# Optimization experiments

Hardware: AMD Instinct MI355X
Metric: run time of the kernel (lower is better)

The kernel has to match this reference:

```python
import jax, jax.numpy as jnp
import numpy as np

B, F, DU, DI, DT = 4096, 50, 128, 256, 768
NU, NI = 200000, 100000
EPS = 1e-5

def _batchnorm(x, gamma, beta):
    # training-mode BatchNorm1d: biased batch statistics
    mu = jnp.mean(x, axis=0)
    var = jnp.mean((x - mu) ** 2, axis=0)
    return gamma * (x - mu) / jnp.sqrt(var + EPS) + beta

def setup_inputs() -> dict:
    key = jax.random.key(0)
    ks = jax.random.split(key, 16)
    inp = {
        "user_id": jax.random.randint(ks[0], (B,), 0, NU),
        "item_id": jax.random.randint(ks[1], (B,), 0, NI),
        "user_follow": jax.random.randint(ks[2], (B, F), 0, NU),
        "follow_len": jax.random.randint(ks[3], (B,), 0, F + 1),
        "feature_item": jax.random.normal(ks[4], (B, 3), dtype=jnp.float32),
        "tag_emb": jax.random.normal(ks[5], (B, DT), dtype=jnp.float32),
        "user_emb_table": jax.random.normal(ks[6], (NU, DU), dtype=jnp.float32) * 0.02,
        "item_emb_table": jax.random.normal(ks[7], (NI, DI), dtype=jnp.float32) * 0.02,
        "fc1_w": jax.random.normal(ks[8], (DI, DT + DI), dtype=jnp.float32) * 0.02,
        "fc1_b": jnp.zeros((DI,), dtype=jnp.float32),
        "fc2_w": jax.random.normal(ks[9], (DU, DU + DI), dtype=jnp.float32) * 0.02,
        "fc2_b": jnp.zeros((DU,), dtype=jnp.float32),
        "out_w": jax.random.normal(ks[10], (1, DU + 3), dtype=jnp.float32) * 0.02,
        "out_b": jnp.zeros((1,), dtype=jnp.float32),
        "bn1_g": jnp.ones((DI,), dtype=jnp.float32),
        "bn1_b": jnp.zeros((DI,), dtype=jnp.float32),
        "bn2_g": jnp.ones((DU,), dtype=jnp.float32),
        "bn2_b": jnp.zeros((DU,), dtype=jnp.float32),
    }
    return inp

def reference(user_id, item_id, user_follow, follow_len, feature_item, tag_emb,
              user_emb_table, item_emb_table, fc1_w, fc1_b, fc2_w, fc2_b,
              out_w, out_b, bn1_g, bn1_b, bn2_g, bn2_b):
    # --- user interaction embedding (vectorized padded attention) ---
    u = user_emb_table[user_id]                       # [B, 128]
    f = user_emb_table[user_follow]                   # [B, F, 128]
    uf = jnp.concatenate([u[:, None, :], f], axis=1)  # [B, 1+F, 128]
    scores = jnp.einsum('bnd,bd->bn', uf, u)          # [B, 1+F]
    pos_valid = jnp.arange(F)[None, :] < follow_len[:, None]
    valid = jnp.concatenate([jnp.ones((user_id.shape[0], 1), dtype=bool), pos_valid], axis=1)
    scores = jnp.where(valid, scores, -1e9)
    w = jax.nn.softmax(scores, axis=1)
    att = jnp.einsum('bn,bnd->bd', w, uf)             # [B, 128]
    user_embedded = jnp.where((follow_len > 1)[:, None], att, u)
    # --- item fusion path ---
    item_embedded = item_emb_table[item_id]           # [B, 256]
    h1 = jnp.concatenate([tag_emb, item_embedded], axis=1) @ fc1_w.T + fc1_b
    item_vector = jax.nn.relu(_batchnorm(h1 + item_embedded, bn1_g, bn1_b))
    h2 = jnp.concatenate([user_embedded, item_vector], axis=1) @ fc2_w.T + fc2_b
    item_user_vector = jax.nn.relu(_batchnorm(h2 + user_embedded, bn2_g, bn2_b))
    logits = jnp.concatenate([item_user_vector, feature_item], axis=1) @ out_w.T + out_b
    return logits
```

## Files before the change

### kernel.cpp

```cpp
#include <hip/hip_runtime.h>
#include <cstdint>
#include <cstddef>

#define BATCH 4096
#define F_FOLLOW 50
#define NROW 51
#define DU 128
#define DI 256
#define DT 768
#define K1 (DT + DI)
#define K2 (DU + DI)
#define EPS 1e-5f

__global__ __launch_bounds__(256) void attn_kernel(
    const int* __restrict__ user_id,
    const int* __restrict__ user_follow,
    const int* __restrict__ follow_len,
    const float* __restrict__ utab,
    float* __restrict__ uemb_out,
    float* __restrict__ zero_region)
{
    __shared__ float uf[NROW * 133];
    __shared__ int   idx[NROW];
    __shared__ float w[NROW];

    const int b   = blockIdx.x;
    const int tid = threadIdx.x;

    if (b == 0)
        for (int i = tid; i < 768; i += 256) zero_region[i] = 0.f;

    const int fl  = follow_len[b];
    const int nv  = fl < F_FOLLOW ? fl : F_FOLLOW;

    if (tid < NROW)
        idx[tid] = (tid == 0) ? user_id[b] : user_follow[b * F_FOLLOW + tid - 1];
    __syncthreads();

    const int nrows = nv + 1;
    for (int e = tid; e < nrows * 32; e += 256) {
        int n = e >> 5, d4 = (e & 31) << 2;
        float4 v = *(const float4*)(utab + (size_t)idx[n] * 128 + d4);
        float* dst = &uf[n * 133 + d4];
        dst[0] = v.x; dst[1] = v.y; dst[2] = v.z; dst[3] = v.w;
    }
    __syncthreads();

    if (tid < 64) {
        int n = (tid <= nv) ? tid : 0;
        float acc = 0.f;
        #pragma unroll 8
        for (int d = 0; d < 128; ++d)
            acc += uf[n * 133 + d] * uf[d];
        float s = (tid <= nv) ? acc : -1e30f;
        float m = s;
        #pragma unroll
        for (int off = 32; off; off >>= 1)
            m = fmaxf(m, __shfl_xor(m, off, 64));
        float e = expf(s - m);
        float l = e;
        #pragma unroll
        for (int off = 32; off; off >>= 1)
            l += __shfl_xor(l, off, 64);
        if (tid < NROW) w[tid] = e / l;
    }
    __syncthreads();

    if (tid < 128) {
        float acc = 0.f;
        for (int n = 0; n <= nv; ++n)
            acc += w[n] * uf[n * 133 + tid];
        float out = (fl > 1) ? acc : uf[tid];
        uemb_out[(size_t)b * DU + tid] = out;
    }
}

__global__ __launch_bounds__(512) void gemm1_kernel(
    const float* __restrict__ tag,
    const int*   __restrict__ item_id,
    const float* __restrict__ itab,
    const float* __restrict__ w1,
    const float* __restrict__ b1,
    float* __restrict__ a1,
    float* __restrict__ gsum,
    float* __restrict__ gsq)
{
    __shared__ float As[32][68];
    __shared__ float Bs[32][68];
    __shared__ int   iid[64];
    __shared__ float lsum[64];
    __shared__ float lsq[64];

    const int tid = threadIdx.x;
    const int m0 = blockIdx.x * 64;
    const int n0 = blockIdx.y * 64;
    if (tid < 64) {
        iid[tid]  = item_id[m0 + tid];
        lsum[tid] = 0.f;
        lsq[tid]  = 0.f;
    }

    const int lr = tid >> 3;
    const int lk = (tid & 7) * 4;
    const int tx = tid & 15;
    const int ty = tid >> 4;

    float acc[2][4] = {};
    __syncthreads();

    for (int kt = 0; kt < K1; kt += 32) {
        float4 av, bv;
        if (kt < DT)
            av = *(const float4*)(tag + (size_t)(m0 + lr) * DT + kt + lk);
        else
            av = *(const float4*)(itab + (size_t)iid[lr] * DI + (kt - DT) + lk);
        bv = *(const float4*)(w1 + (size_t)(n0 + lr) * K1 + kt + lk);

        __syncthreads();
        As[lk + 0][lr] = av.x; As[lk + 1][lr] = av.y;
        As[lk + 2][lr] = av.z; As[lk + 3][lr] = av.w;
        Bs[lk + 0][lr] = bv.x; Bs[lk + 1][lr] = bv.y;
        Bs[lk + 2][lr] = bv.z; Bs[lk + 3][lr] = bv.w;
        __syncthreads();

        #pragma unroll
        for (int k = 0; k < 32; ++k) {
            float2 a2v = *(const float2*)&As[k][ty * 2];
            float4 b4  = *(const float4*)&Bs[k][tx * 4];
            float a[2]  = {a2v.x, a2v.y};
            float bb[4] = {b4.x, b4.y, b4.z, b4.w};
            #pragma unroll
            for (int i = 0; i < 2; ++i)
                #pragma unroll
                for (int j = 0; j < 4; ++j)
                    acc[i][j] += a[i] * bb[j];
        }
    }

    float s[4] = {0.f, 0.f, 0.f, 0.f};
    float q[4] = {0.f, 0.f, 0.f, 0.f};
    #pragma unroll
    for (int i = 0; i < 2; ++i) {
        int lrow = ty * 2 + i;
        int row  = m0 + lrow;
        int ii   = iid[lrow];
        #pragma unroll
        for (int j = 0; j < 4; ++j) {
            int col = n0 + tx * 4 + j;
            float v = acc[i][j] + b1[col] + itab[(size_t)ii * DI + col];
            a1[(size_t)row * DI + col] = v;
            s[j] += v;
            q[j] += v * v;
        }
    }
    #pragma unroll
    for (int j = 0; j < 4; ++j) {
        atomicAdd(&lsum[tx * 4 + j], s[j]);
        atomicAdd(&lsq [tx * 4 + j], q[j]);
    }
    __syncthreads();
    if (tid < 64) {
        atomicAdd(&gsum[n0 + tid], lsum[tid]);
        atomicAdd(&gsq [n0 + tid], lsq [tid]);
    }
}

__global__ __launch_bounds__(256) void gemm2_kernel(
    const float* __restrict__ uemb,
    const float* __restrict__ a1,
    const float* __restrict__ gsum1,
    const float* __restrict__ gsq1,
    const float* __restrict__ g1,
    const float* __restrict__ bb1,
    const float* __restrict__ w2,
    const float* __restrict__ b2,
    float* __restrict__ a2,
    float* __restrict__ gsum,
    float* __restrict__ gsq)
{
    __shared__ float As[32][36];
    __shared__ float Bs[32][68];
    __shared__ __align__(16) float sc1s[256];
    __shared__ __align__(16) float sh1s[256];
    __shared__ float lsum[64];
    __shared__ float lsq[64];

    const int tid = threadIdx.x;
    const int m0 = blockIdx.x * 32;
    const int n0 = blockIdx.y * 64;

    {
        float mean = gsum1[tid] * (1.f / 4096.f);
        float var  = gsq1[tid] * (1.f / 4096.f) - mean * mean;
        var = fmaxf(var, 0.f);
        float sc = g1[tid] / sqrtf(var + EPS);
        sc1s[tid] = sc;
        sh1s[tid] = bb1[tid] - mean * sc;
    }
    if (tid < 64) { lsum[tid] = 0.f; lsq[tid] = 0.f; }

    const int ar = tid >> 3;
    const int ak = (tid & 7) * 4;
    const int br = tid >> 2;
    const int bk = (tid & 3) * 8;
    const int tx = tid & 15;
    const int ty = tid >> 4;

    float acc[2][4] = {};
    __syncthreads();

    for (int kt = 0; kt < K2; kt += 32) {
        float4 av;
        int row = m0 + ar;
        if (kt < DU) {
            av = *(const float4*)(uemb + (size_t)row * DU + kt + ak);
        } else {
            int c = kt + ak - DU;
            float4 v  = *(const float4*)(a1 + (size_t)row * DI + c);
            float4 sv = *(const float4*)(sc1s + c);
            float4 hv = *(const float4*)(sh1s + c);
            av.x = fmaxf(v.x * sv.x + hv.x, 0.f);
            av.y = fmaxf(v.y * sv.y + hv.y, 0.f);
            av.z = fmaxf(v.z * sv.z + hv.z, 0.f);
            av.w = fmaxf(v.w * sv.w + hv.w, 0.f);
        }
        const float* wrow = w2 + (size_t)(n0 + br) * K2 + kt + bk;
        float4 bv0 = *(const float4*)(wrow);
        float4 bv1 = *(const float4*)(wrow + 4);

        __syncthreads();
        As[ak + 0][ar] = av.x; As[ak + 1][ar] = av.y;
        As[ak + 2][ar] = av.z; As[ak + 3][ar] = av.w;
        Bs[bk + 0][br] = bv0.x; Bs[bk + 1][br] = bv0.y;
        Bs[bk + 2][br] = bv0.z; Bs[bk + 3][br] = bv0.w;
        Bs[bk + 4][br] = bv1.x; Bs[bk + 5][br] = bv1.y;
        Bs[bk + 6][br] = bv1.z; Bs[bk + 7][br] = bv1.w;
        __syncthreads();

        #pragma unroll
        for (int k = 0; k < 32; ++k) {
            float2 a2v = *(const float2*)&As[k][ty * 2];
            float4 b4  = *(const float4*)&Bs[k][tx * 4];
            float a[2]  = {a2v.x, a2v.y};
            float bb[4] = {b4.x, b4.y, b4.z, b4.w};
            #pragma unroll
            for (int i = 0; i < 2; ++i)
                #pragma unroll
                for (int j = 0; j < 4; ++j)
                    acc[i][j] += a[i] * bb[j];
        }
    }

    float s[4] = {0.f, 0.f, 0.f, 0.f};
    float q[4] = {0.f, 0.f, 0.f, 0.f};
    #pragma unroll
    for (int i = 0; i < 2; ++i) {
        int row = m0 + ty * 2 + i;
        #pragma unroll
        for (int j = 0; j < 4; ++j) {
            int col = n0 + tx * 4 + j;
            float v = acc[i][j] + b2[col] + uemb[(size_t)row * DU + col];
            a2[(size_t)row * DU + col] = v;
            s[j] += v;
            q[j] += v * v;
        }
    }
    #pragma unroll
    for (int j = 0; j < 4; ++j) {
        atomicAdd(&lsum[tx * 4 + j], s[j]);
        atomicAdd(&lsq [tx * 4 + j], q[j]);
    }
    __syncthreads();
    if (tid < 64) {
        atomicAdd(&gsum[n0 + tid], lsum[tid]);
        atomicAdd(&gsq [n0 + tid], lsq [tid]);
    }
}

__global__ __launch_bounds__(256) void final_kernel(
    const float* __restrict__ a2,
    const float* __restrict__ gsum2,
    const float* __restrict__ gsq2,
    const float* __restrict__ g2,
    const float* __restrict__ bb2,
    const float* __restrict__ feat,
    const float* __restrict__ ow, const float* __restrict__ ob,
    float* __restrict__ out)
{
    __shared__ float sc2s[128];
    __shared__ float sh2s[128];

    const int tid  = threadIdx.x;
    if (tid < 128) {
        float mean = gsum2[tid] * (1.f / 4096.f);
        float var  = gsq2[tid] * (1.f / 4096.f) - mean * mean;
        var = fmaxf(var, 0.f);
        float sc = g2[tid] / sqrtf(var + EPS);
        sc2s[tid] = sc;
        sh2s[tid] = bb2[tid] - mean * sc;
    }
    __syncthreads();

    const int lane = tid & 63;
    const int wv   = tid >> 6;
    const int b    = blockIdx.x * 4 + wv;

    float acc = 0.f;
    #pragma unroll
    for (int h = 0; h < 2; ++h) {
        int j = lane + h * 64;
        float v = fmaxf(a2[(size_t)b * DU + j] * sc2s[j] + sh2s[j], 0.f);
        acc += v * ow[j];
    }
    #pragma unroll
    for (int off = 32; off; off >>= 1)
        acc += __shfl_xor(acc, off, 64);
    if (lane == 0) {
        acc += feat[(size_t)b * 3 + 0] * ow[128]
             + feat[(size_t)b * 3 + 1] * ow[129]
             + feat[(size_t)b * 3 + 2] * ow[130]
             + ob[0];
        out[b] = acc;
    }
}

extern "C" void kernel_launch(void* const* d_in, const int* in_sizes, int n_in,
                              void* d_out, int out_size, void* d_ws, size_t ws_size,
                              hipStream_t stream)
{
    const int*   user_id = (const int*)d_in[0];
    const int*   item_id = (const int*)d_in[1];
    const int*   ufollow = (const int*)d_in[2];
    const int*   flen    = (const int*)d_in[3];
    const float* feat    = (const float*)d_in[4];
    const float* tag     = (const float*)d_in[5];
    const float* utab    = (const float*)d_in[6];
    const float* itab    = (const float*)d_in[7];
    const float* w1      = (const float*)d_in[8];
    const float* b1      = (const float*)d_in[9];
    const float* w2      = (const float*)d_in[10];
    const float* b2      = (const float*)d_in[11];
    const float* ow      = (const float*)d_in[12];
    const float* ob      = (const float*)d_in[13];
    const float* g1      = (const float*)d_in[14];
    const float* bb1     = (const float*)d_in[15];
    const float* g2      = (const float*)d_in[16];
    const float* bb2     = (const float*)d_in[17];

    float* ws     = (float*)d_ws;
    float* uemb   = ws;
    float* a1     = uemb + BATCH * DU;
    float* a2     = a1 + BATCH * DI;
    float* sum1   = a2 + BATCH * DU;
    float* sumsq1 = sum1 + 256;
    float* sum2   = sumsq1 + 256;
    float* sumsq2 = sum2 + 128;

    attn_kernel<<<BATCH, 256, 0, stream>>>(user_id, ufollow, flen, utab, uemb,
                                           sum1);
    gemm1_kernel<<<dim3(64, 4), 512, 0, stream>>>(tag, item_id, itab, w1, b1, a1,
                                                  sum1, sumsq1);
    gemm2_kernel<<<dim3(128, 2), 256, 0, stream>>>(uemb, a1, sum1, sumsq1, g1, bb1,
                                                   w2, b2, a2, sum2, sumsq2);
    final_kernel<<<1024, 256, 0, stream>>>(a2, sum2, sumsq2, g2, bb2, feat, ow, ob,
                                           (float*)d_out);
}
```

Before: 317.3 us.

## Use split-bf16 MFMA for both GEMMs and parallelize attention scoring

Both FC GEMMs now split each fp32 operand into high and low bf16 halves and run three 16x16x32 bf16 MFMA products per tile, replacing the scalar FMA inner loops. Global loads for the next K slice are register-prefetched while the current slice is converted. gemm2's row tile grows from 32 to 64 rows, and gemm1 drops from 512 to 256 threads. The attention kernel spreads the score dot products over all 256 threads and splits the weighted sum across two halves, at the cost of extra conversion arithmetic and a small loss of precision versus true fp32.

```diff
diff --git a/kernel.cpp b/kernel.cpp
--- a/kernel.cpp
+++ b/kernel.cpp
@@ -11,6 +11,29 @@
 #define K1 (DT + DI)
 #define K2 (DU + DI)
 #define EPS 1e-5f
+
+typedef float f32x4 __attribute__((ext_vector_type(4)));
+typedef short s16x8 __attribute__((ext_vector_type(8)));
+
+#define MFMA16(a, b, c) __builtin_amdgcn_mfma_f32_16x16x32_bf16(a, b, c, 0, 0, 0)
+
+__device__ __forceinline__ unsigned rne16(float r) {
+    unsigned b = __float_as_uint(r);
+    return (b + 0x7FFFu + ((b >> 16) & 1u)) >> 16;
+}
+__device__ __forceinline__ void cvt4(float4 v, unsigned &h0, unsigned &h1,
+                                     unsigned &l0, unsigned &l1) {
+    unsigned bx = __float_as_uint(v.x), by = __float_as_uint(v.y);
+    unsigned bz = __float_as_uint(v.z), bw = __float_as_uint(v.w);
+    h0 = (bx >> 16) | (by & 0xFFFF0000u);
+    h1 = (bz >> 16) | (bw & 0xFFFF0000u);
+    float rx = v.x - __uint_as_float(bx & 0xFFFF0000u);
+    float ry = v.y - __uint_as_float(by & 0xFFFF0000u);
+    float rz = v.z - __uint_as_float(bz & 0xFFFF0000u);
+    float rw = v.w - __uint_as_float(bw & 0xFFFF0000u);
+    l0 = rne16(rx) | (rne16(ry) << 16);
+    l1 = rne16(rz) | (rne16(rw) << 16);
+}
 
 __global__ __launch_bounds__(256) void attn_kernel(
     const int* __restrict__ user_id,
@@ -23,6 +46,8 @@
     __shared__ float uf[NROW * 133];
     __shared__ int   idx[NROW];
     __shared__ float w[NROW];
+    __shared__ float sArr[64];
+    __shared__ float pacc[256];
 
     const int b   = blockIdx.x;
     const int tid = threadIdx.x;
@@ -30,8 +55,8 @@
     if (b == 0)
         for (int i = tid; i < 768; i += 256) zero_region[i] = 0.f;
 
-    const int fl  = follow_len[b];
-    const int nv  = fl < F_FOLLOW ? fl : F_FOLLOW;
+    const int fl = follow_len[b];
+    const int nv = fl < F_FOLLOW ? fl : F_FOLLOW;
 
     if (tid < NROW)
         idx[tid] = (tid == 0) ? user_id[b] : user_follow[b * F_FOLLOW + tid - 1];
@@ -46,13 +71,25 @@
     }
     __syncthreads();
 
+    {
+        int n = tid >> 2, q = tid & 3;
+        float acc = 0.f;
+        if (n <= nv) {
+            int d0 = q * 32;
+            #pragma unroll 8
+            for (int dd = 0; dd < 32; ++dd) {
+                int d = d0 + ((dd + q * 8) & 31);
+                acc += uf[n * 133 + d] * uf[d];
+            }
+        }
+        acc += __shfl_xor(acc, 1);
+        acc += __shfl_xor(acc, 2);
+        if (q == 0 && n <= nv) sArr[n] = acc;
+    }
+    __syncthreads();
+
     if (tid < 64) {
-        int n = (tid <= nv) ? tid : 0;
-        float acc = 0.f;
-        #pragma unroll 8
-        for (int d = 0; d < 128; ++d)
-            acc += uf[n * 133 + d] * uf[d];
-        float s = (tid <= nv) ? acc : -1e30f;
+        float s = (tid <= nv) ? sArr[tid] : -1e30f;
         float m = s;
         #pragma unroll
         for (int off = 32; off; off >>= 1)
@@ -62,20 +99,26 @@
         #pragma unroll
         for (int off = 32; off; off >>= 1)
             l += __shfl_xor(l, off, 64);
-        if (tid < NROW) w[tid] = e / l;
-    }
-    __syncthreads();
-
+        if (tid <= nv) w[tid] = e / l;
+    }
+    __syncthreads();
+
+    {
+        int d = tid & 127, half = tid >> 7;
+        float o = 0.f;
+        for (int n = half; n <= nv; n += 2)
+            o += w[n] * uf[n * 133 + d];
+        pacc[tid] = o;
+    }
+    __syncthreads();
     if (tid < 128) {
-        float acc = 0.f;
-        for (int n = 0; n <= nv; ++n)
-            acc += w[n] * uf[n * 133 + tid];
-        float out = (fl > 1) ? acc : uf[tid];
-        uemb_out[(size_t)b * DU + tid] = out;
-    }
-}
-
-__global__ __launch_bounds__(512) void gemm1_kernel(
+        float o = pacc[tid] + pacc[tid + 128];
+        float outv = (fl > 1) ? o : uf[tid];
+        uemb_out[(size_t)b * DU + tid] = outv;
+    }
+}
+
+__global__ __launch_bounds__(256) void gemm1_kernel(
     const float* __restrict__ tag,
     const int*   __restrict__ item_id,
     const float* __restrict__ itab,
@@ -85,78 +128,104 @@
     float* __restrict__ gsum,
     float* __restrict__ gsq)
 {
-    __shared__ float As[32][68];
-    __shared__ float Bs[32][68];
+    __shared__ __align__(16) unsigned short Ah[64][40], Al[64][40];
+    __shared__ __align__(16) unsigned short Bh[64][40], Bl[64][40];
     __shared__ int   iid[64];
-    __shared__ float lsum[64];
-    __shared__ float lsq[64];
+    __shared__ float lsum[64], lsq[64];
 
     const int tid = threadIdx.x;
     const int m0 = blockIdx.x * 64;
     const int n0 = blockIdx.y * 64;
-    if (tid < 64) {
-        iid[tid]  = item_id[m0 + tid];
-        lsum[tid] = 0.f;
-        lsq[tid]  = 0.f;
-    }
-
-    const int lr = tid >> 3;
-    const int lk = (tid & 7) * 4;
-    const int tx = tid & 15;
-    const int ty = tid >> 4;
-
-    float acc[2][4] = {};
+
+    if (tid < 64) { iid[tid] = item_id[m0 + tid]; lsum[tid] = 0.f; lsq[tid] = 0.f; }
+
+    const int r  = tid >> 2;
+    const int k8 = (tid & 3) * 8;
+
+    const int w  = tid >> 6;
+    const int l  = tid & 63;
+    const int wr = (w >> 1) * 32;
+    const int wc = (w & 1) * 32;
+    const int fr = l & 15;
+    const int fk = (l >> 4) * 8;
+
+    f32x4 acc00 = {}, acc01 = {}, acc10 = {}, acc11 = {};
+
+    float4 ra0, ra1, rb0, rb1;
+    {
+        const float* ap = tag + (size_t)(m0 + r) * DT + k8;
+        ra0 = *(const float4*)ap;  ra1 = *(const float4*)(ap + 4);
+        const float* bp = w1 + (size_t)(n0 + r) * K1 + k8;
+        rb0 = *(const float4*)bp;  rb1 = *(const float4*)(bp + 4);
+    }
     __syncthreads();
 
     for (int kt = 0; kt < K1; kt += 32) {
-        float4 av, bv;
-        if (kt < DT)
-            av = *(const float4*)(tag + (size_t)(m0 + lr) * DT + kt + lk);
-        else
-            av = *(const float4*)(itab + (size_t)iid[lr] * DI + (kt - DT) + lk);
-        bv = *(const float4*)(w1 + (size_t)(n0 + lr) * K1 + kt + lk);
-
+        if (kt) __syncthreads();
+
+        unsigned h0, h1, h2, h3, l0, l1, l2, l3;
+        cvt4(ra0, h0, h1, l0, l1); cvt4(ra1, h2, h3, l2, l3);
+        *(uint4*)&Ah[r][k8] = make_uint4(h0, h1, h2, h3);
+        *(uint4*)&Al[r][k8] = make_uint4(l0, l1, l2, l3);
+        cvt4(rb0, h0, h1, l0, l1); cvt4(rb1, h2, h3, l2, l3);
+        *(uint4*)&Bh[r][k8] = make_uint4(h0, h1, h2, h3);
+        *(uint4*)&Bl[r][k8] = make_uint4(l0, l1, l2, l3);
+
+        if (kt + 32 < K1) {
+            const int kn = kt + 32;
+            const float* ap;
+            if (kn < DT) ap = tag + (size_t)(m0 + r) * DT + kn + k8;
+            else         ap = itab + (size_t)iid[r] * DI + (kn - DT) + k8;
+            ra0 = *(const float4*)ap;  ra1 = *(const float4*)(ap + 4);
+            const float* bp = w1 + (size_t)(n0 + r) * K1 + kn + k8;
+            rb0 = *(const float4*)bp;  rb1 = *(const float4*)(bp + 4);
+        }
         __syncthreads();
-        As[lk + 0][lr] = av.x; As[lk + 1][lr] = av.y;
-        As[lk + 2][lr] = av.z; As[lk + 3][lr] = av.w;
-        Bs[lk + 0][lr] = bv.x; Bs[lk + 1][lr] = bv.y;
-        Bs[lk + 2][lr] = bv.z; Bs[lk + 3][lr] = bv.w;
-        __syncthreads();
-
+
+        s16x8 ah0 = *(const s16x8*)&Ah[wr + fr][fk];
+        s16x8 ah1 = *(const s16x8*)&Ah[wr + 16 + fr][fk];
+        s16x8 al0 = *(const s16x8*)&Al[wr + fr][fk];
+        s16x8 al1 = *(const s16x8*)&Al[wr + 16 + fr][fk];
+        s16x8 bh0 = *(const s16x8*)&Bh[wc + fr][fk];
+        s16x8 bh1 = *(const s16x8*)&Bh[wc + 16 + fr][fk];
+        s16x8 bl0 = *(const s16x8*)&Bl[wc + fr][fk];
+        s16x8 bl1 = *(const s16x8*)&Bl[wc + 16 + fr][fk];
+
+        acc00 = MFMA16(ah0, bh0, acc00);
+        acc01 = MFMA16(ah0, bh1, acc01);
+        acc10 = MFMA16(ah1, bh0, acc10);
+        acc11 = MFMA16(ah1, bh1, acc11);
+        acc00 = MFMA16(ah0, bl0, acc00);
+        acc01 = MFMA16(ah0, bl1, acc01);
+        acc10 = MFMA16(ah1, bl0, acc10);
+        acc11 = MFMA16(ah1, bl1, acc11);
+        acc00 = MFMA16(al0, bh0, acc00);
+        acc01 = MFMA16(al0, bh1, acc01);
+        acc10 = MFMA16(al1, bh0, acc10);
+        acc11 = MFMA16(al1, bh1, acc11);
+    }
+
+    const f32x4 accs[2][2] = {{acc00, acc01}, {acc10, acc11}};
+    #pragma unroll
+    for (int ct = 0; ct < 2; ++ct) {
+        int cg  = wc + ct * 16 + fr;
+        int col = n0 + cg;
+        float bias = b1[col];
+        float s_ = 0.f, q_ = 0.f;
         #pragma unroll
-        for (int k = 0; k < 32; ++k) {
-            float2 a2v = *(const float2*)&As[k][ty * 2];
-            float4 b4  = *(const float4*)&Bs[k][tx * 4];
-            float a[2]  = {a2v.x, a2v.y};
-            float bb[4] = {b4.x, b4.y, b4.z, b4.w};
+        for (int rt = 0; rt < 2; ++rt) {
+            int rb = wr + rt * 16 + ((l >> 4) << 2);
             #pragma unroll
-            for (int i = 0; i < 2; ++i)
-                #pragma unroll
-                for (int j = 0; j < 4; ++j)
-                    acc[i][j] += a[i] * bb[j];
+            for (int i = 0; i < 4; ++i) {
+                int rl = rb + i;
+                float v = accs[rt][ct][i] + bias + itab[(size_t)iid[rl] * DI + col];
+                a1[(size_t)(m0 + rl) * DI + col] = v;
+                s_ += v; q_ += v * v;
+            }
         }
-    }
-
-    float s[4] = {0.f, 0.f, 0.f, 0.f};
-    float q[4] = {0.f, 0.f, 0.f, 0.f};
-    #pragma unroll
-    for (int i = 0; i < 2; ++i) {
-        int lrow = ty * 2 + i;
-        int row  = m0 + lrow;
-        int ii   = iid[lrow];
-        #pragma unroll
-        for (int j = 0; j < 4; ++j) {
-            int col = n0 + tx * 4 + j;
-            float v = acc[i][j] + b1[col] + itab[(size_t)ii * DI + col];
-            a1[(size_t)row * DI + col] = v;
-            s[j] += v;
-            q[j] += v * v;
-        }
-    }
-    #pragma unroll
-    for (int j = 0; j < 4; ++j) {
-        atomicAdd(&lsum[tx * 4 + j], s[j]);
-        atomicAdd(&lsq [tx * 4 + j], q[j]);
+        s_ += __shfl_xor(s_, 16); s_ += __shfl_xor(s_, 32);
+        q_ += __shfl_xor(q_, 16); q_ += __shfl_xor(q_, 32);
+        if (l < 16) { atomicAdd(&lsum[cg], s_); atomicAdd(&lsq[cg], q_); }
     }
     __syncthreads();
     if (tid < 64) {
@@ -178,15 +247,13 @@
     float* __restrict__ gsum,
     float* __restrict__ gsq)
 {
-    __shared__ float As[32][36];
-    __shared__ float Bs[32][68];
-    __shared__ __align__(16) float sc1s[256];
-    __shared__ __align__(16) float sh1s[256];
-    __shared__ float lsum[64];
-    __shared__ float lsq[64];
+    __shared__ __align__(16) unsigned short Ah[64][40], Al[64][40];
+    __shared__ __align__(16) unsigned short Bh[64][40], Bl[64][40];
+    __shared__ __align__(16) float sc1s[256], sh1s[256];
+    __shared__ float lsum[64], lsq[64];
 
     const int tid = threadIdx.x;
-    const int m0 = blockIdx.x * 32;
+    const int m0 = blockIdx.x * 64;
     const int n0 = blockIdx.y * 64;
 
     {
@@ -199,76 +266,108 @@
     }
     if (tid < 64) { lsum[tid] = 0.f; lsq[tid] = 0.f; }
 
-    const int ar = tid >> 3;
-    const int ak = (tid & 7) * 4;
-    const int br = tid >> 2;
-    const int bk = (tid & 3) * 8;
-    const int tx = tid & 15;
-    const int ty = tid >> 4;
-
-    float acc[2][4] = {};
+    const int r  = tid >> 2;
+    const int k8 = (tid & 3) * 8;
+    const int w  = tid >> 6;
+    const int l  = tid & 63;
+    const int wr = (w >> 1) * 32;
+    const int wc = (w & 1) * 32;
+    const int fr = l & 15;
+    const int fk = (l >> 4) * 8;
+
+    f32x4 acc00 = {}, acc01 = {}, acc10 = {}, acc11 = {};
+
+    float4 ra0, ra1, rb0, rb1;
+    {
+        const float* ap = uemb + (size_t)(m0 + r) * DU + k8;
+        ra0 = *(const float4*)ap;  ra1 = *(const float4*)(ap + 4);
+        const float* bp = w2 + (size_t)(n0 + r) * K2 + k8;
+        rb0 = *(const float4*)bp;  rb1 = *(const float4*)(bp + 4);
+    }
     __syncthreads();
 
     for (int kt = 0; kt < K2; kt += 32) {
-        float4 av;
-        int row = m0 + ar;
-        if (kt < DU) {
-            av = *(const float4*)(uemb + (size_t)row * DU + kt + ak);
-        } else {
-            int c = kt + ak - DU;
-            float4 v  = *(const float4*)(a1 + (size_t)row * DI + c);
-            float4 sv = *(const float4*)(sc1s + c);
-            float4 hv = *(const float4*)(sh1s + c);
-            av.x = fmaxf(v.x * sv.x + hv.x, 0.f);
-            av.y = fmaxf(v.y * sv.y + hv.y, 0.f);
-            av.z = fmaxf(v.z * sv.z + hv.z, 0.f);
-            av.w = fmaxf(v.w * sv.w + hv.w, 0.f);
+        if (kt) __syncthreads();
+
+        unsigned h0, h1, h2, h3, l0, l1, l2, l3;
+        cvt4(ra0, h0, h1, l0, l1); cvt4(ra1, h2, h3, l2, l3);
+        *(uint4*)&Ah[r][k8] = make_uint4(h0, h1, h2, h3);
+        *(uint4*)&Al[r][k8] = make_uint4(l0, l1, l2, l3);
+        cvt4(rb0, h0, h1, l0, l1); cvt4(rb1, h2, h3, l2, l3);
+        *(uint4*)&Bh[r][k8] = make_uint4(h0, h1, h2, h3);
+        *(uint4*)&Bl[r][k8] = make_uint4(l0, l1, l2, l3);
+
+        if (kt + 32 < K2) {
+            const int kn = kt + 32;
+            if (kn < DU) {
+                const float* ap = uemb + (size_t)(m0 + r) * DU + kn + k8;
+                ra0 = *(const float4*)ap;  ra1 = *(const float4*)(ap + 4);
+            } else {
+                int c = kn + k8 - DU;
+                float4 v0 = *(const float4*)(a1 + (size_t)(m0 + r) * DI + c);
+                float4 v1 = *(const float4*)(a1 + (size_t)(m0 + r) * DI + c + 4);
+                float4 s0 = *(const float4*)&sc1s[c];
+                float4 s1 = *(const float4*)&sc1s[c + 4];
+                float4 h0v = *(const float4*)&sh1s[c];
+                float4 h1v = *(const float4*)&sh1s[c + 4];
+                ra0.x = fmaxf(v0.x * s0.x + h0v.x, 0.f);
+                ra0.y = fmaxf(v0.y * s0.y + h0v.y, 0.f);
+                ra0.z = fmaxf(v0.z * s0.z + h0v.z, 0.f);
+                ra0.w = fmaxf(v0.w * s0.w + h0v.w, 0.f);
+                ra1.x = fmaxf(v1.x * s1.x + h1v.x, 0.f);
+                ra1.y = fmaxf(v1.y * s1.y + h1v.y, 0.f);
+                ra1.z = fmaxf(v1.z * s1.z + h1v.z, 0.f);
+                ra1.w = fmaxf(v1.w * s1.w + h1v.w, 0.f);
+            }
+            const float* bp = w2 + (size_t)(n0 + r) * K2 + kn + k8;
+            rb0 = *(const float4*)bp;  rb1 = *(const float4*)(bp + 4);
         }
-        const float* wrow = w2 + (size_t)(n0 + br) * K2 + kt + bk;
-        float4 bv0 = *(const float4*)(wrow);
-        float4 bv1 = *(const float4*)(wrow + 4);
-
         __syncthreads();
-        As[ak + 0][ar] = av.x; As[ak + 1][ar] = av.y;
-        As[ak + 2][ar] = av.z; As[ak + 3][ar] = av.w;
-        Bs[bk + 0][br] = bv0.x; Bs[bk + 1][br] = bv0.y;
-        Bs[bk + 2][br] = bv0.z; Bs[bk + 3][br] = bv0.w;
-        Bs[bk + 4][br] = bv1.x; Bs[bk + 5][br] = bv1.y;
-        Bs[bk + 6][br] = bv1.z; Bs[bk + 7][br] = bv1.w;
-        __syncthreads();
-
+
+        s16x8 ah0 = *(const s16x8*)&Ah[wr + fr][fk];
+        s16x8 ah1 = *(const s16x8*)&Ah[wr + 16 + fr][fk];
+        s16x8 al0 = *(const s16x8*)&Al[wr + fr][fk];
+        s16x8 al1 = *(const s16x8*)&Al[wr + 16 + fr][fk];
+        s16x8 bh0 = *(const s16x8*)&Bh[wc + fr][fk];
+        s16x8 bh1 = *(const s16x8*)&Bh[wc + 16 + fr][fk];
+        s16x8 bl0 = *(const s16x8*)&Bl[wc + fr][fk];
+        s16x8 bl1 = *(const s16x8*)&Bl[wc + 16 + fr][fk];
+
+        acc00 = MFMA16(ah0, bh0, acc00);
+        acc01 = MFMA16(ah0, bh1, acc01);
+        acc10 = MFMA16(ah1, bh0, acc10);
+        acc11 = MFMA16(ah1, bh1, acc11);
+        acc00 = MFMA16(ah0, bl0, acc00);
+        acc01 = MFMA16(ah0, bl1, acc01);
+        acc10 = MFMA16(ah1, bl0, acc10);
+        acc11 = MFMA16(ah1, bl1, acc11);
+        acc00 = MFMA16(al0, bh0, acc00);
+        acc01 = MFMA16(al0, bh1, acc01);
+        acc10 = MFMA16(al1, bh0, acc10);
+        acc11 = MFMA16(al1, bh1, acc11);
+    }
+
+    const f32x4 accs[2][2] = {{acc00, acc01}, {acc10, acc11}};
+    #pragma unroll
+    for (int ct = 0; ct < 2; ++ct) {
+        int cg  = wc + ct * 16 + fr;
+        int col = n0 + cg;
+        float bias = b2[col];
+        float s_ = 0.f, q_ = 0.f;
         #pragma unroll
-        for (int k = 0; k < 32; ++k) {
-            float2 a2v = *(const float2*)&As[k][ty * 2];
-            float4 b4  = *(const float4*)&Bs[k][tx * 4];
-            float a[2]  = {a2v.x, a2v.y};
-            float bb[4] = {b4.x, b4.y, b4.z, b4.w};
+        for (int rt = 0; rt < 2; ++rt) {
+            int rb = wr + rt * 16 + ((l >> 4) << 2);
             #pragma unroll
-            for (int i = 0; i < 2; ++i)
-                #pragma unroll
-                for (int j = 0; j < 4; ++j)
-                    acc[i][j] += a[i] * bb[j];
+            for (int i = 0; i < 4; ++i) {
+                int rl = rb + i;
+                float v = accs[rt][ct][i] + bias + uemb[(size_t)(m0 + rl) * DU + col];
+                a2[(size_t)(m0 + rl) * DU + col] = v;
+                s_ += v; q_ += v * v;
+            }
         }
-    }
-
-    float s[4] = {0.f, 0.f, 0.f, 0.f};
-    float q[4] = {0.f, 0.f, 0.f, 0.f};
-    #pragma unroll
-    for (int i = 0; i < 2; ++i) {
-        int row = m0 + ty * 2 + i;
-        #pragma unroll
-        for (int j = 0; j < 4; ++j) {
-            int col = n0 + tx * 4 + j;
-            float v = acc[i][j] + b2[col] + uemb[(size_t)row * DU + col];
-            a2[(size_t)row * DU + col] = v;
-            s[j] += v;
-            q[j] += v * v;
-        }
-    }
-    #pragma unroll
-    for (int j = 0; j < 4; ++j) {
-        atomicAdd(&lsum[tx * 4 + j], s[j]);
-        atomicAdd(&lsq [tx * 4 + j], q[j]);
+        s_ += __shfl_xor(s_, 16); s_ += __shfl_xor(s_, 32);
+        q_ += __shfl_xor(q_, 16); q_ += __shfl_xor(q_, 32);
+        if (l < 16) { atomicAdd(&lsum[cg], s_); atomicAdd(&lsq[cg], q_); }
     }
     __syncthreads();
     if (tid < 64) {
@@ -358,10 +457,10 @@
 
     attn_kernel<<<BATCH, 256, 0, stream>>>(user_id, ufollow, flen, utab, uemb,
                                            sum1);
-    gemm1_kernel<<<dim3(64, 4), 512, 0, stream>>>(tag, item_id, itab, w1, b1, a1,
+    gemm1_kernel<<<dim3(64, 4), 256, 0, stream>>>(tag, item_id, itab, w1, b1, a1,
                                                   sum1, sumsq1);
-    gemm2_kernel<<<dim3(128, 2), 256, 0, stream>>>(uemb, a1, sum1, sumsq1, g1, bb1,
-                                                   w2, b2, a2, sum2, sumsq2);
+    gemm2_kernel<<<dim3(64, 2), 256, 0, stream>>>(uemb, a1, sum1, sumsq1, g1, bb1,
+                                                  w2, b2, a2, sum2, sumsq2);
     final_kernel<<<1024, 256, 0, stream>>>(a2, sum2, sumsq2, g2, bb2, feat, ow, ob,
                                            (float*)d_out);
 }
```

Result: faster. 283.0 us (-10.8%).
